# Performance work log

Hardware: AMD Instinct MI355X
Metric: run time of the kernel (lower is better)

## Reference

```python
import jax, jax.numpy as jnp
import numpy as np

B, T, D, MP = 32, 256, 512, 20


def setup_inputs() -> dict:
    key = jax.random.key(0)
    k1, k2, k3 = jax.random.split(key, 3)
    reps_lt = jax.random.normal(k1, (B, T, D), dtype=jnp.float32)
    reps_rt = jax.random.normal(k2, (B, T, D), dtype=jnp.float32)
    kernel = jax.random.normal(k3, (1, 1, 1, MP, D), dtype=jnp.float32)
    return {"reps_lt": reps_lt, "reps_rt": reps_rt, "kernel": kernel}


def reference(reps_lt, reps_rt, kernel):
    # kernel: (1,1,1,m,d) -> (m,d)
    km = kernel.reshape(kernel.shape[-2], kernel.shape[-1])
    # scores[b,t,s,m] = sum_d lt[b,t,d] * km[m,d] * rt[b,s,d]
    # matches original broadcast-multiply + sum over d (cosine_norm=False path)
    scores = jnp.einsum('btd,md,bsd->btsm', reps_lt, km, reps_rt)
    match = jnp.tanh(scores)               # [b, t1, t2, m]
    return jnp.max(match, axis=2)          # max-pool over t2 -> [b, t1, m]
```

## Files before the change

kernel.cpp:

```cpp
#include <hip/hip_runtime.h>


constexpr int TT = 256;
constexpr int DD = 512;
constexpr int NM = 20;
constexpr int NB = 32;
constexpr int BM = 128;
constexpr int BN = 256;
constexpr int BK = 32;
constexpr int NK = DD / BK;

typedef short bf16x8 __attribute__((ext_vector_type(8)));
typedef float f32x4  __attribute__((ext_vector_type(4)));

__device__ __forceinline__ void async_ld16(const void* g, void* l) {
    __builtin_amdgcn_global_load_lds(
        (const __attribute__((address_space(1))) void*)g,
        (__attribute__((address_space(3))) void*)l, 16, 0, 0);
}

__device__ __forceinline__ unsigned pack_bf16(float lo, float hi) {
    unsigned ulo = __builtin_bit_cast(unsigned, lo);
    unsigned uhi = __builtin_bit_cast(unsigned, hi);
    return (ulo >> 16) | (uhi & 0xFFFF0000u);
}

__device__ __forceinline__ unsigned mulpack(unsigned a2, float k0, float k1) {
    float f0 = __builtin_bit_cast(float, a2 << 16) * k0;
    float f1 = __builtin_bit_cast(float, a2 & 0xFFFF0000u) * k1;
    return __builtin_amdgcn_perm(__builtin_bit_cast(unsigned, f1),
                                 __builtin_bit_cast(unsigned, f0), 0x07060302u);
}

__global__ __launch_bounds__(256)
void cast_bf16(const float* __restrict__ lt, const float* __restrict__ rt,
               unsigned short* __restrict__ ltb, unsigned short* __restrict__ rtb)
{
    const int half = (int)gridDim.x >> 1;
    int bid = blockIdx.x;
    const float* src;
    unsigned short* dst;
    if (bid < half) { src = lt; dst = ltb; }
    else            { src = rt; dst = rtb; bid -= half; }
    size_t base = ((size_t)bid * 256 + threadIdx.x) * 8;
    float4 a = *(const float4*)(src + base);
    float4 b = *(const float4*)(src + base + 4);
    uint4 w;
    w.x = pack_bf16(a.x, a.y);
    w.y = pack_bf16(a.z, a.w);
    w.z = pack_bf16(b.x, b.y);
    w.w = pack_bf16(b.z, b.w);
    *(uint4*)(dst + base) = w;
}

__global__ __launch_bounds__(256, 2)
void mp_match_main(const unsigned short* __restrict__ ltb, const unsigned short* __restrict__ rtb,
                   const float* __restrict__ km, float* __restrict__ out)
{
    __shared__ __attribute__((aligned(16))) unsigned short Bsh[2][BN * 4 * 8];
    __shared__ __attribute__((aligned(16))) unsigned short Ash[2][BM * 4 * 8];
    __shared__ __attribute__((aligned(16))) float kmf[DD];
    __shared__ __attribute__((aligned(16))) float maxbuf[2][BM];

    const int f = blockIdx.x;
    const int c8 = f & 7;
    const int i = f >> 3;
    const int b = c8 + 8 * (i / 40);
    const int j = i % 40;
    const int m = j >> 1;
    const int t0 = (j & 1) * BM;

    const int tid  = threadIdx.x;
    const int w    = tid >> 6;
    const int lane = tid & 63;
    const int l15  = lane & 15;
    const int l4   = lane >> 4;
    const int wt   = (w & 1) * 64;
    const int wsi  = w >> 1;

    kmf[tid]       = km[(size_t)m * DD + tid];
    kmf[tid + 256] = km[(size_t)m * DD + tid + 256];

    const unsigned short* ltB = ltb + ((size_t)b * TT + t0) * DD;
    const unsigned short* rtB = rtb + (size_t)b * TT * DD;

    const int ar0 = tid >> 2,        ac = tid & 3;
    const int ar1 = (tid + 256) >> 2;
    const int ap0 = ac ^ ((ar0 >> 1) & 3);
    const int ap1 = ac ^ ((ar1 >> 1) & 3);
    const unsigned short* aSrc0 = ltB + (size_t)ar0 * DD + ac * 8;
    const unsigned short* aSrc1 = ltB + (size_t)ar1 * DD + ac * 8;

    auto issueB = [&](int kk, int buf) {
        const int kb = kk * BK;
#pragma unroll
        for (int q = 0; q < 4; ++q) {
            int slot = q * 256 + tid;
            int row = slot >> 2;
            int c = (slot & 3) ^ ((slot >> 3) & 3);
            async_ld16(rtB + (size_t)row * DD + kb + c * 8,
                       (char*)&Bsh[buf][0] + (size_t)slot * 16);
        }
    };
    auto aload = [&](int kk, uint4* ar) {
        ar[0] = *(const uint4*)(aSrc0 + kk * BK);
        ar[1] = *(const uint4*)(aSrc1 + kk * BK);
    };
    auto scaleWrite = [&](int kk, int buf, const uint4* ar) {
        float4 k0 = *(const float4*)&kmf[kk * BK + ac * 8];
        float4 k1 = *(const float4*)&kmf[kk * BK + ac * 8 + 4];
        uint4 o;
        o.x = mulpack(ar[0].x, k0.x, k0.y);
        o.y = mulpack(ar[0].y, k0.z, k0.w);
        o.z = mulpack(ar[0].z, k1.x, k1.y);
        o.w = mulpack(ar[0].w, k1.z, k1.w);
        *(uint4*)&Ash[buf][(size_t)(ar0 * 4 + ap0) * 8] = o;
        o.x = mulpack(ar[1].x, k0.x, k0.y);
        o.y = mulpack(ar[1].y, k0.z, k0.w);
        o.z = mulpack(ar[1].z, k1.x, k1.y);
        o.w = mulpack(ar[1].w, k1.z, k1.w);
        *(uint4*)&Ash[buf][(size_t)(ar1 * 4 + ap1) * 8] = o;
    };

    f32x4 acc[4][8] = {};
    uint4 ar[2];

    aload(0, ar);
    issueB(0, 0);
    __syncthreads();
    scaleWrite(0, 0, ar);

    const int fpos = l4 ^ ((l15 >> 1) & 3);

    for (int kk = 0; kk < NK; ++kk) {
        const int buf = kk & 1;
        __syncthreads();
        if (kk + 1 < NK) {
            aload(kk + 1, ar);
            issueB(kk + 1, buf ^ 1);
        }
        bf16x8 af[4], bv[8];
#pragma unroll
        for (int ii = 0; ii < 4; ++ii)
            af[ii] = *(const bf16x8*)&Ash[buf][(size_t)((wt + ii * 16 + l15) * 4 + fpos) * 8];
#pragma unroll
        for (int jj = 0; jj < 8; ++jj)
            bv[jj] = *(const bf16x8*)&Bsh[buf][(size_t)((wsi * 128 + jj * 16 + l15) * 4 + fpos) * 8];
#pragma unroll
        for (int ii = 0; ii < 4; ++ii)
#pragma unroll
            for (int jj = 0; jj < 8; ++jj)
                acc[ii][jj] = __builtin_amdgcn_mfma_f32_16x16x32_bf16(af[ii], bv[jj], acc[ii][jj], 0, 0, 0);
        if (kk + 1 < NK)
            scaleWrite(kk + 1, buf ^ 1, ar);
    }

#pragma unroll
    for (int ii = 0; ii < 4; ++ii) {
        f32x4 v = acc[ii][0];
#pragma unroll
        for (int jj = 1; jj < 8; ++jj) {
            v.x = fmaxf(v.x, acc[ii][jj].x);
            v.y = fmaxf(v.y, acc[ii][jj].y);
            v.z = fmaxf(v.z, acc[ii][jj].z);
            v.w = fmaxf(v.w, acc[ii][jj].w);
        }
#pragma unroll
        for (int off = 1; off < 16; off <<= 1) {
            v.x = fmaxf(v.x, __shfl_xor(v.x, off, 64));
            v.y = fmaxf(v.y, __shfl_xor(v.y, off, 64));
            v.z = fmaxf(v.z, __shfl_xor(v.z, off, 64));
            v.w = fmaxf(v.w, __shfl_xor(v.w, off, 64));
        }
        if (l15 == 0)
            *(f32x4*)&maxbuf[wsi][wt + ii * 16 + l4 * 4] = v;
    }
    __syncthreads();
    if (tid < BM) {
        float v = fmaxf(maxbuf[0][tid], maxbuf[1][tid]);
        out[((size_t)b * TT + t0 + tid) * NM + m] = tanhf(v);
    }
}

__global__ __launch_bounds__(256, 2)
void mp_match_kernel(const float* __restrict__ lt, const float* __restrict__ rt,
                     const float* __restrict__ km, float* __restrict__ out)
{
    __shared__ __attribute__((aligned(16))) unsigned short Ash[2][4][BM][8];
    __shared__ __attribute__((aligned(16))) unsigned short Bsh2[2][4][BN][8];
    __shared__ __attribute__((aligned(16))) float maxbuf[2][BM];

    const int ttile = blockIdx.x, m = blockIdx.y, b = blockIdx.z;
    const int t0 = ttile * BM;
    const int tid = threadIdx.x, wave = tid >> 6, lane = tid & 63;
    const int l15 = lane & 15, l4 = lane >> 4;
    const int wt = (wave & 1) * 64, wsi = wave >> 1;

    const float* ltp = lt + ((size_t)b * TT + t0) * DD;
    const float* rtp = rt + (size_t)b * TT * DD;
    const float* kmp = km + (size_t)m * DD;
    const int a_t = tid >> 1, a_h = tid & 1;

    f32x4 acc[4][8] = {};

    auto stage = [&](int kk, int buf) {
        const int d0 = kk * BK;
        const float* ap = ltp + (size_t)a_t * DD + d0 + a_h * 16;
        const float* kp = kmp + d0 + a_h * 16;
#pragma unroll
        for (int q = 0; q < 2; ++q) {
            float4 x0 = *(const float4*)(ap + q * 8);
            float4 x1 = *(const float4*)(ap + q * 8 + 4);
            float4 k0 = *(const float4*)(kp + q * 8);
            float4 k1 = *(const float4*)(kp + q * 8 + 4);
            uint4 wv;
            wv.x = pack_bf16(x0.x * k0.x, x0.y * k0.y);
            wv.y = pack_bf16(x0.z * k0.z, x0.w * k0.w);
            wv.z = pack_bf16(x1.x * k1.x, x1.y * k1.y);
            wv.w = pack_bf16(x1.z * k1.z, x1.w * k1.w);
            *(uint4*)&Ash[buf][a_h * 2 + q][a_t][0] = wv;
        }
        const float* bp = rtp + (size_t)tid * DD + d0;
#pragma unroll
        for (int p = 0; p < 4; ++p) {
            float4 y0 = *(const float4*)(bp + p * 8);
            float4 y1 = *(const float4*)(bp + p * 8 + 4);
            uint4 wv;
            wv.x = pack_bf16(y0.x, y0.y);
            wv.y = pack_bf16(y0.z, y0.w);
            wv.z = pack_bf16(y1.x, y1.y);
            wv.w = pack_bf16(y1.z, y1.w);
            *(uint4*)&Bsh2[buf][p][tid][0] = wv;
        }
    };

    stage(0, 0);
    for (int kk = 0; kk < NK; ++kk) {
        const int buf = kk & 1;
        __syncthreads();
        bf16x8 af[4], bfv[8];
#pragma unroll
        for (int i = 0; i < 4; ++i)
            af[i] = *(const bf16x8*)&Ash[buf][l4][wt + i * 16 + l15][0];
#pragma unroll
        for (int j = 0; j < 8; ++j)
            bfv[j] = *(const bf16x8*)&Bsh2[buf][l4][wsi * 128 + j * 16 + l15][0];
        if (kk + 1 < NK) stage(kk + 1, buf ^ 1);
#pragma unroll
        for (int i = 0; i < 4; ++i)
#pragma unroll
            for (int j = 0; j < 8; ++j)
                acc[i][j] = __builtin_amdgcn_mfma_f32_16x16x32_bf16(af[i], bfv[j], acc[i][j], 0, 0, 0);
    }
#pragma unroll
    for (int i = 0; i < 4; ++i) {
        f32x4 v = acc[i][0];
#pragma unroll
        for (int j = 1; j < 8; ++j) {
            v.x = fmaxf(v.x, acc[i][j].x); v.y = fmaxf(v.y, acc[i][j].y);
            v.z = fmaxf(v.z, acc[i][j].z); v.w = fmaxf(v.w, acc[i][j].w);
        }
#pragma unroll
        for (int off = 1; off < 16; off <<= 1) {
            v.x = fmaxf(v.x, __shfl_xor(v.x, off, 64));
            v.y = fmaxf(v.y, __shfl_xor(v.y, off, 64));
            v.z = fmaxf(v.z, __shfl_xor(v.z, off, 64));
            v.w = fmaxf(v.w, __shfl_xor(v.w, off, 64));
        }
        if (l15 == 0) *(f32x4*)&maxbuf[wsi][wt + i * 16 + l4 * 4] = v;
    }
    __syncthreads();
    if (tid < BM) {
        float v = fmaxf(maxbuf[0][tid], maxbuf[1][tid]);
        out[((size_t)b * TT + t0 + tid) * NM + m] = tanhf(v);
    }
}

extern "C" void kernel_launch(void* const* d_in, const int* in_sizes, int n_in,
                              void* d_out, int out_size, void* d_ws, size_t ws_size,
                              hipStream_t stream) {
    const float* lt  = (const float*)d_in[0];
    const float* rt  = (const float*)d_in[1];
    const float* km  = (const float*)d_in[2];
    float*       out = (float*)d_out;

    const size_t elems = (size_t)NB * TT * DD;
    const size_t need  = 2 * elems * sizeof(unsigned short);

    if (ws_size >= need) {
        unsigned short* ltb = (unsigned short*)d_ws;
        unsigned short* rtb = ltb + elems;
        const int cast_blocks_per_tensor = (int)(elems / (8 * 256));
        cast_bf16<<<cast_blocks_per_tensor * 2, 256, 0, stream>>>(lt, rt, ltb, rtb);
        mp_match_main<<<dim3(1280), 256, 0, stream>>>(ltb, rtb, km, out);
    } else {
        mp_match_kernel<<<dim3(TT / BM, NM, NB), 256, 0, stream>>>(lt, rt, km, out);
    }
}
```

Measured before the change: 133.6 us.

## Split s-dimension across two blocks with partial max buffer and combine kernel

Adds a split kernel that tiles the s axis into two 128-row halves, so each block computes a 128x128 tile with smaller LDS and fewer accumulators, launching 2560 blocks at occupancy 3. Partial maxima go to a workspace buffer, and a small combine kernel takes the max of the two halves and applies tanh. The aim is more parallelism and occupancy. The cost is an extra kernel launch, a partial-result write and read, and duplicate A-tile loads and scaling per block.

```diff
diff --git a/kernel.cpp b/kernel.cpp
--- a/kernel.cpp
+++ b/kernel.cpp
@@ -53,22 +53,24 @@
     *(uint4*)(dst + base) = w;
 }
 
-__global__ __launch_bounds__(256, 2)
-void mp_match_main(const unsigned short* __restrict__ ltb, const unsigned short* __restrict__ rtb,
-                   const float* __restrict__ km, float* __restrict__ out)
+__global__ __launch_bounds__(256, 3)
+void mp_match_split(const unsigned short* __restrict__ ltb, const unsigned short* __restrict__ rtb,
+                    const float* __restrict__ km, float* __restrict__ part)
 {
-    __shared__ __attribute__((aligned(16))) unsigned short Bsh[2][BN * 4 * 8];
     __shared__ __attribute__((aligned(16))) unsigned short Ash[2][BM * 4 * 8];
+    __shared__ __attribute__((aligned(16))) unsigned short Bsh[2][BM * 4 * 8];
     __shared__ __attribute__((aligned(16))) float kmf[DD];
     __shared__ __attribute__((aligned(16))) float maxbuf[2][BM];
 
-    const int f = blockIdx.x;
+    const int f  = blockIdx.x;
     const int c8 = f & 7;
-    const int i = f >> 3;
-    const int b = c8 + 8 * (i / 40);
-    const int j = i % 40;
-    const int m = j >> 1;
-    const int t0 = (j & 1) * BM;
+    const int i  = f >> 3;
+    const int b  = c8 + 8 * (i / 80);
+    const int j  = i % 80;
+    const int m  = j >> 2;
+    const int t0 = ((j >> 1) & 1) * 128;
+    const int s0 = (j & 1) * 128;
+    const int sT = j & 1;
 
     const int tid  = threadIdx.x;
     const int w    = tid >> 6;
@@ -76,13 +78,13 @@
     const int l15  = lane & 15;
     const int l4   = lane >> 4;
     const int wt   = (w & 1) * 64;
-    const int wsi  = w >> 1;
+    const int wsO  = (w >> 1) * 64;
 
     kmf[tid]       = km[(size_t)m * DD + tid];
     kmf[tid + 256] = km[(size_t)m * DD + tid + 256];
 
     const unsigned short* ltB = ltb + ((size_t)b * TT + t0) * DD;
-    const unsigned short* rtB = rtb + (size_t)b * TT * DD;
+    const unsigned short* rtB = rtb + ((size_t)b * TT + s0) * DD;
 
     const int ar0 = tid >> 2,        ac = tid & 3;
     const int ar1 = (tid + 256) >> 2;
@@ -94,7 +96,7 @@
     auto issueB = [&](int kk, int buf) {
         const int kb = kk * BK;
 #pragma unroll
-        for (int q = 0; q < 4; ++q) {
+        for (int q = 0; q < 2; ++q) {
             int slot = q * 256 + tid;
             int row = slot >> 2;
             int c = (slot & 3) ^ ((slot >> 3) & 3);
@@ -122,6 +124,143 @@
         *(uint4*)&Ash[buf][(size_t)(ar1 * 4 + ap1) * 8] = o;
     };
 
+    f32x4 acc[4][4] = {};
+    uint4 ar[2];
+
+    aload(0, ar);
+    issueB(0, 0);
+    __syncthreads();
+    scaleWrite(0, 0, ar);
+
+    const int fpos = l4 ^ ((l15 >> 1) & 3);
+
+    for (int kk = 0; kk < NK; ++kk) {
+        const int buf = kk & 1;
+        __syncthreads();
+        if (kk + 1 < NK) {
+            aload(kk + 1, ar);
+            issueB(kk + 1, buf ^ 1);
+        }
+        bf16x8 af[4], bv[4];
+#pragma unroll
+        for (int ii = 0; ii < 4; ++ii)
+            af[ii] = *(const bf16x8*)&Ash[buf][(size_t)((wt + ii * 16 + l15) * 4 + fpos) * 8];
+#pragma unroll
+        for (int jj = 0; jj < 4; ++jj)
+            bv[jj] = *(const bf16x8*)&Bsh[buf][(size_t)((wsO + jj * 16 + l15) * 4 + fpos) * 8];
+#pragma unroll
+        for (int ii = 0; ii < 4; ++ii)
+#pragma unroll
+            for (int jj = 0; jj < 4; ++jj)
+                acc[ii][jj] = __builtin_amdgcn_mfma_f32_16x16x32_bf16(af[ii], bv[jj], acc[ii][jj], 0, 0, 0);
+        if (kk + 1 < NK)
+            scaleWrite(kk + 1, buf ^ 1, ar);
+    }
+
+#pragma unroll
+    for (int ii = 0; ii < 4; ++ii) {
+        f32x4 v = acc[ii][0];
+#pragma unroll
+        for (int jj = 1; jj < 4; ++jj) {
+            v.x = fmaxf(v.x, acc[ii][jj].x);
+            v.y = fmaxf(v.y, acc[ii][jj].y);
+            v.z = fmaxf(v.z, acc[ii][jj].z);
+            v.w = fmaxf(v.w, acc[ii][jj].w);
+        }
+#pragma unroll
+        for (int off = 1; off < 16; off <<= 1) {
+            v.x = fmaxf(v.x, __shfl_xor(v.x, off, 64));
+            v.y = fmaxf(v.y, __shfl_xor(v.y, off, 64));
+            v.z = fmaxf(v.z, __shfl_xor(v.z, off, 64));
+            v.w = fmaxf(v.w, __shfl_xor(v.w, off, 64));
+        }
+        if (l15 == 0)
+            *(f32x4*)&maxbuf[w >> 1][wt + ii * 16 + l4 * 4] = v;
+    }
+    __syncthreads();
+    if (tid < BM) {
+        float v = fmaxf(maxbuf[0][tid], maxbuf[1][tid]);
+        part[(((size_t)sT * NB + b) * TT + t0 + tid) * NM + m] = v;
+    }
+}
+
+__global__ __launch_bounds__(256)
+void mp_combine(const float* __restrict__ part, float* __restrict__ out, int n)
+{
+    int idx = blockIdx.x * 256 + threadIdx.x;
+    if (idx < n)
+        out[idx] = tanhf(fmaxf(part[idx], part[(size_t)n + idx]));
+}
+
+__global__ __launch_bounds__(256, 2)
+void mp_match_main(const unsigned short* __restrict__ ltb, const unsigned short* __restrict__ rtb,
+                   const float* __restrict__ km, float* __restrict__ out)
+{
+    __shared__ __attribute__((aligned(16))) unsigned short Bsh[2][BN * 4 * 8];
+    __shared__ __attribute__((aligned(16))) unsigned short Ash[2][BM * 4 * 8];
+    __shared__ __attribute__((aligned(16))) float kmf[DD];
+    __shared__ __attribute__((aligned(16))) float maxbuf[2][BM];
+
+    const int f = blockIdx.x;
+    const int c8 = f & 7;
+    const int i = f >> 3;
+    const int b = c8 + 8 * (i / 40);
+    const int j = i % 40;
+    const int m = j >> 1;
+    const int t0 = (j & 1) * BM;
+
+    const int tid  = threadIdx.x;
+    const int w    = tid >> 6;
+    const int lane = tid & 63;
+    const int l15  = lane & 15;
+    const int l4   = lane >> 4;
+    const int wt   = (w & 1) * 64;
+    const int wsi  = w >> 1;
+
+    kmf[tid]       = km[(size_t)m * DD + tid];
+    kmf[tid + 256] = km[(size_t)m * DD + tid + 256];
+
+    const unsigned short* ltB = ltb + ((size_t)b * TT + t0) * DD;
+    const unsigned short* rtB = rtb + (size_t)b * TT * DD;
+
+    const int ar0 = tid >> 2,        ac = tid & 3;
+    const int ar1 = (tid + 256) >> 2;
+    const int ap0 = ac ^ ((ar0 >> 1) & 3);
+    const int ap1 = ac ^ ((ar1 >> 1) & 3);
+    const unsigned short* aSrc0 = ltB + (size_t)ar0 * DD + ac * 8;
+    const unsigned short* aSrc1 = ltB + (size_t)ar1 * DD + ac * 8;
+
+    auto issueB = [&](int kk, int buf) {
+        const int kb = kk * BK;
+#pragma unroll
+        for (int q = 0; q < 4; ++q) {
+            int slot = q * 256 + tid;
+            int row = slot >> 2;
+            int c = (slot & 3) ^ ((slot >> 3) & 3);
+            async_ld16(rtB + (size_t)row * DD + kb + c * 8,
+                       (char*)&Bsh[buf][0] + (size_t)slot * 16);
+        }
+    };
+    auto aload = [&](int kk, uint4* ar) {
+        ar[0] = *(const uint4*)(aSrc0 + kk * BK);
+        ar[1] = *(const uint4*)(aSrc1 + kk * BK);
+    };
+    auto scaleWrite = [&](int kk, int buf, const uint4* ar) {
+        float4 k0 = *(const float4*)&kmf[kk * BK + ac * 8];
+        float4 k1 = *(const float4*)&kmf[kk * BK + ac * 8 + 4];
+        uint4 o;
+        o.x = mulpack(ar[0].x, k0.x, k0.y);
+        o.y = mulpack(ar[0].y, k0.z, k0.w);
+        o.z = mulpack(ar[0].z, k1.x, k1.y);
+        o.w = mulpack(ar[0].w, k1.z, k1.w);
+        *(uint4*)&Ash[buf][(size_t)(ar0 * 4 + ap0) * 8] = o;
+        o.x = mulpack(ar[1].x, k0.x, k0.y);
+        o.y = mulpack(ar[1].y, k0.z, k0.w);
+        o.z = mulpack(ar[1].z, k1.x, k1.y);
+        o.w = mulpack(ar[1].w, k1.z, k1.w);
+        *(uint4*)&Ash[buf][(size_t)(ar1 * 4 + ap1) * 8] = o;
+    };
+
     f32x4 acc[4][8] = {};
     uint4 ar[2];
 
@@ -285,14 +424,22 @@
     float*       out = (float*)d_out;
 
     const size_t elems = (size_t)NB * TT * DD;
-    const size_t need  = 2 * elems * sizeof(unsigned short);
-
-    if (ws_size >= need) {
+    const size_t castB = 2 * elems * sizeof(unsigned short);
+    const int    nOut  = NB * TT * NM;
+    const size_t partB = 2 * (size_t)nOut * sizeof(float);
+
+    if (ws_size >= castB + partB) {
         unsigned short* ltb = (unsigned short*)d_ws;
         unsigned short* rtb = ltb + elems;
-        const int cast_blocks_per_tensor = (int)(elems / (8 * 256));
-        cast_bf16<<<cast_blocks_per_tensor * 2, 256, 0, stream>>>(lt, rt, ltb, rtb);
-        mp_match_main<<<dim3(1280), 256, 0, stream>>>(ltb, rtb, km, out);
+        float* part = (float*)((char*)d_ws + castB);
+        cast_bf16<<<4096, 256, 0, stream>>>(lt, rt, ltb, rtb);
+        mp_match_split<<<2560, 256, 0, stream>>>(ltb, rtb, km, part);
+        mp_combine<<<(nOut + 255) / 256, 256, 0, stream>>>(part, out, nOut);
+    } else if (ws_size >= castB) {
+        unsigned short* ltb = (unsigned short*)d_ws;
+        unsigned short* rtb = ltb + elems;
+        cast_bf16<<<4096, 256, 0, stream>>>(lt, rt, ltb, rtb);
+        mp_match_main<<<1280, 256, 0, stream>>>(ltb, rtb, km, out);
     } else {
         mp_match_kernel<<<dim3(TT / BM, NM, NB), 256, 0, stream>>>(lt, rt, km, out);
     }
```

Result: no change. 133.0 us (-0.4%).

## Halve M tile to 64 rows and raise occupancy to three blocks per CU

Applied to the files above, without the earlier changes.

Shrinks the lt row tile from 128 to 64, which doubles the grid to 2560 blocks. Each wave now owns a 64x64 output sub-tile (4x4 MFMA accumulators) instead of 64x128, and the final max reduces over four waves. Launch bounds are raised to 3 blocks per CU to use the lower register and LDS footprint. The goal is better latency hiding and load balance across CUs. The cost is that every rt tile is streamed twice as often and there are fewer MFMAs per LDS read.

```diff
diff --git a/kernel.cpp b/kernel.cpp
--- a/kernel.cpp
+++ b/kernel.cpp
@@ -5,7 +5,7 @@
 constexpr int DD = 512;
 constexpr int NM = 20;
 constexpr int NB = 32;
-constexpr int BM = 128;
+constexpr int BM = 64;
 constexpr int BN = 256;
 constexpr int BK = 32;
 constexpr int NK = DD / BK;
@@ -53,30 +53,29 @@
     *(uint4*)(dst + base) = w;
 }
 
-__global__ __launch_bounds__(256, 2)
+__global__ __launch_bounds__(256, 3)
 void mp_match_main(const unsigned short* __restrict__ ltb, const unsigned short* __restrict__ rtb,
                    const float* __restrict__ km, float* __restrict__ out)
 {
     __shared__ __attribute__((aligned(16))) unsigned short Bsh[2][BN * 4 * 8];
     __shared__ __attribute__((aligned(16))) unsigned short Ash[2][BM * 4 * 8];
     __shared__ __attribute__((aligned(16))) float kmf[DD];
-    __shared__ __attribute__((aligned(16))) float maxbuf[2][BM];
-
-    const int f = blockIdx.x;
+    __shared__ __attribute__((aligned(16))) float maxbuf[4][BM];
+
+    const int f  = blockIdx.x;
     const int c8 = f & 7;
-    const int i = f >> 3;
-    const int b = c8 + 8 * (i / 40);
-    const int j = i % 40;
-    const int m = j >> 1;
-    const int t0 = (j & 1) * BM;
+    const int i  = f >> 3;
+    const int b  = c8 + 8 * (i / 80);
+    const int j  = i % 80;
+    const int m  = j >> 2;
+    const int t0 = (j & 3) * BM;
 
     const int tid  = threadIdx.x;
     const int w    = tid >> 6;
     const int lane = tid & 63;
     const int l15  = lane & 15;
     const int l4   = lane >> 4;
-    const int wt   = (w & 1) * 64;
-    const int wsi  = w >> 1;
+    const int wsO  = w * 64;
 
     kmf[tid]       = km[(size_t)m * DD + tid];
     kmf[tid + 256] = km[(size_t)m * DD + tid + 256];
@@ -84,12 +83,9 @@
     const unsigned short* ltB = ltb + ((size_t)b * TT + t0) * DD;
     const unsigned short* rtB = rtb + (size_t)b * TT * DD;
 
-    const int ar0 = tid >> 2,        ac = tid & 3;
-    const int ar1 = (tid + 256) >> 2;
-    const int ap0 = ac ^ ((ar0 >> 1) & 3);
-    const int ap1 = ac ^ ((ar1 >> 1) & 3);
-    const unsigned short* aSrc0 = ltB + (size_t)ar0 * DD + ac * 8;
-    const unsigned short* aSrc1 = ltB + (size_t)ar1 * DD + ac * 8;
+    const int arow = tid >> 2, ac = tid & 3;
+    const int apos = ac ^ ((arow >> 1) & 3);
+    const unsigned short* aSrc = ltB + (size_t)arow * DD + ac * 8;
 
     auto issueB = [&](int kk, int buf) {
         const int kb = kk * BK;
@@ -102,30 +98,21 @@
                        (char*)&Bsh[buf][0] + (size_t)slot * 16);
         }
     };
-    auto aload = [&](int kk, uint4* ar) {
-        ar[0] = *(const uint4*)(aSrc0 + kk * BK);
-        ar[1] = *(const uint4*)(aSrc1 + kk * BK);
-    };
-    auto scaleWrite = [&](int kk, int buf, const uint4* ar) {
+    auto scaleWrite = [&](int kk, int buf, uint4 a) {
         float4 k0 = *(const float4*)&kmf[kk * BK + ac * 8];
         float4 k1 = *(const float4*)&kmf[kk * BK + ac * 8 + 4];
         uint4 o;
-        o.x = mulpack(ar[0].x, k0.x, k0.y);
-        o.y = mulpack(ar[0].y, k0.z, k0.w);
-        o.z = mulpack(ar[0].z, k1.x, k1.y);
-        o.w = mulpack(ar[0].w, k1.z, k1.w);
-        *(uint4*)&Ash[buf][(size_t)(ar0 * 4 + ap0) * 8] = o;
-        o.x = mulpack(ar[1].x, k0.x, k0.y);
-        o.y = mulpack(ar[1].y, k0.z, k0.w);
-        o.z = mulpack(ar[1].z, k1.x, k1.y);
-        o.w = mulpack(ar[1].w, k1.z, k1.w);
-        *(uint4*)&Ash[buf][(size_t)(ar1 * 4 + ap1) * 8] = o;
+        o.x = mulpack(a.x, k0.x, k0.y);
+        o.y = mulpack(a.y, k0.z, k0.w);
+        o.z = mulpack(a.z, k1.x, k1.y);
+        o.w = mulpack(a.w, k1.z, k1.w);
+        *(uint4*)&Ash[buf][(size_t)(arow * 4 + apos) * 8] = o;
     };
 
-    f32x4 acc[4][8] = {};
-    uint4 ar[2];
-
-    aload(0, ar);
+    f32x4 acc[4][4] = {};
+    uint4 ar;
+
+    ar = *(const uint4*)(aSrc);
     issueB(0, 0);
     __syncthreads();
     scaleWrite(0, 0, ar);
@@ -136,20 +123,20 @@
         const int buf = kk & 1;
         __syncthreads();
         if (kk + 1 < NK) {
-            aload(kk + 1, ar);
+            ar = *(const uint4*)(aSrc + (kk + 1) * BK);
             issueB(kk + 1, buf ^ 1);
         }
-        bf16x8 af[4], bv[8];
+        bf16x8 af[4], bv[4];
 #pragma unroll
         for (int ii = 0; ii < 4; ++ii)
-            af[ii] = *(const bf16x8*)&Ash[buf][(size_t)((wt + ii * 16 + l15) * 4 + fpos) * 8];
-#pragma unroll
-        for (int jj = 0; jj < 8; ++jj)
-            bv[jj] = *(const bf16x8*)&Bsh[buf][(size_t)((wsi * 128 + jj * 16 + l15) * 4 + fpos) * 8];
+            af[ii] = *(const bf16x8*)&Ash[buf][(size_t)((ii * 16 + l15) * 4 + fpos) * 8];
+#pragma unroll
+        for (int jj = 0; jj < 4; ++jj)
+            bv[jj] = *(const bf16x8*)&Bsh[buf][(size_t)((wsO + jj * 16 + l15) * 4 + fpos) * 8];
 #pragma unroll
         for (int ii = 0; ii < 4; ++ii)
 #pragma unroll
-            for (int jj = 0; jj < 8; ++jj)
+            for (int jj = 0; jj < 4; ++jj)
                 acc[ii][jj] = __builtin_amdgcn_mfma_f32_16x16x32_bf16(af[ii], bv[jj], acc[ii][jj], 0, 0, 0);
         if (kk + 1 < NK)
             scaleWrite(kk + 1, buf ^ 1, ar);
@@ -159,7 +146,7 @@
     for (int ii = 0; ii < 4; ++ii) {
         f32x4 v = acc[ii][0];
 #pragma unroll
-        for (int jj = 1; jj < 8; ++jj) {
+        for (int jj = 1; jj < 4; ++jj) {
             v.x = fmaxf(v.x, acc[ii][jj].x);
             v.y = fmaxf(v.y, acc[ii][jj].y);
             v.z = fmaxf(v.z, acc[ii][jj].z);
@@ -173,11 +160,12 @@
             v.w = fmaxf(v.w, __shfl_xor(v.w, off, 64));
         }
         if (l15 == 0)
-            *(f32x4*)&maxbuf[wsi][wt + ii * 16 + l4 * 4] = v;
+            *(f32x4*)&maxbuf[w][ii * 16 + l4 * 4] = v;
     }
     __syncthreads();
     if (tid < BM) {
-        float v = fmaxf(maxbuf[0][tid], maxbuf[1][tid]);
+        float v = fmaxf(fmaxf(maxbuf[0][tid], maxbuf[1][tid]),
+                        fmaxf(maxbuf[2][tid], maxbuf[3][tid]));
         out[((size_t)b * TT + t0 + tid) * NM + m] = tanhf(v);
     }
 }
@@ -186,12 +174,12 @@
 void mp_match_kernel(const float* __restrict__ lt, const float* __restrict__ rt,
                      const float* __restrict__ km, float* __restrict__ out)
 {
-    __shared__ __attribute__((aligned(16))) unsigned short Ash[2][4][BM][8];
+    __shared__ __attribute__((aligned(16))) unsigned short Ash[2][4][128][8];
     __shared__ __attribute__((aligned(16))) unsigned short Bsh2[2][4][BN][8];
-    __shared__ __attribute__((aligned(16))) float maxbuf[2][BM];
+    __shared__ __attribute__((aligned(16))) float maxbuf[2][128];
 
     const int ttile = blockIdx.x, m = blockIdx.y, b = blockIdx.z;
-    const int t0 = ttile * BM;
+    const int t0 = ttile * 128;
     const int tid = threadIdx.x, wave = tid >> 6, lane = tid & 63;
     const int l15 = lane & 15, l4 = lane >> 4;
     const int wt = (wave & 1) * 64, wsi = wave >> 1;
@@ -270,7 +258,7 @@
         if (l15 == 0) *(f32x4*)&maxbuf[wsi][wt + i * 16 + l4 * 4] = v;
     }
     __syncthreads();
-    if (tid < BM) {
+    if (tid < 128) {
         float v = fmaxf(maxbuf[0][tid], maxbuf[1][tid]);
         out[((size_t)b * TT + t0 + tid) * NM + m] = tanhf(v);
     }
@@ -285,15 +273,14 @@
     float*       out = (float*)d_out;
 
     const size_t elems = (size_t)NB * TT * DD;
-    const size_t need  = 2 * elems * sizeof(unsigned short);
-
-    if (ws_size >= need) {
+    const size_t castB = 2 * elems * sizeof(unsigned short);
+
+    if (ws_size >= castB) {
         unsigned short* ltb = (unsigned short*)d_ws;
         unsigned short* rtb = ltb + elems;
-        const int cast_blocks_per_tensor = (int)(elems / (8 * 256));
-        cast_bf16<<<cast_blocks_per_tensor * 2, 256, 0, stream>>>(lt, rt, ltb, rtb);
-        mp_match_main<<<dim3(1280), 256, 0, stream>>>(ltb, rtb, km, out);
+        cast_bf16<<<4096, 256, 0, stream>>>(lt, rt, ltb, rtb);
+        mp_match_main<<<2560, 256, 0, stream>>>(ltb, rtb, km, out);
     } else {
-        mp_match_kernel<<<dim3(TT / BM, NM, NB), 256, 0, stream>>>(lt, rt, km, out);
-    }
-}
+        mp_match_kernel<<<dim3(2, NM, NB), 256, 0, stream>>>(lt, rt, km, out);
+    }
+}
```

After: 139.6 us. 4.5% more time.

## Split s-dimension across blocks and combine partial maxima in separate kernel

Applied to the files above, without the earlier changes.

The main matmul-max kernel now tiles the s (rt) dimension in halves of 128, doubling the grid to 2560 smaller blocks with a 4x4 accumulator tile per wave and launch bounds raised to 4 blocks per CU. Partial maxima go to workspace and a new combine kernel takes the max of the two halves and applies tanh. This aims for more occupancy and better load balance across CUs. In exchange the A tile and its per-m scaling are loaded and computed twice, MFMA reuse per LDS load drops, and there is an extra launch and workspace round trip.

```diff
diff --git a/kernel.cpp b/kernel.cpp
--- a/kernel.cpp
+++ b/kernel.cpp
@@ -6,7 +6,6 @@
 constexpr int NM = 20;
 constexpr int NB = 32;
 constexpr int BM = 128;
-constexpr int BN = 256;
 constexpr int BK = 32;
 constexpr int NK = DD / BK;
 
@@ -53,22 +52,24 @@
     *(uint4*)(dst + base) = w;
 }
 
-__global__ __launch_bounds__(256, 2)
-void mp_match_main(const unsigned short* __restrict__ ltb, const unsigned short* __restrict__ rtb,
-                   const float* __restrict__ km, float* __restrict__ out)
+__global__ __launch_bounds__(256, 4)
+void mp_match_split(const unsigned short* __restrict__ ltb, const unsigned short* __restrict__ rtb,
+                    const float* __restrict__ km, float* __restrict__ part)
 {
-    __shared__ __attribute__((aligned(16))) unsigned short Bsh[2][BN * 4 * 8];
     __shared__ __attribute__((aligned(16))) unsigned short Ash[2][BM * 4 * 8];
+    __shared__ __attribute__((aligned(16))) unsigned short Bsh[2][BM * 4 * 8];
     __shared__ __attribute__((aligned(16))) float kmf[DD];
     __shared__ __attribute__((aligned(16))) float maxbuf[2][BM];
 
-    const int f = blockIdx.x;
+    const int f  = blockIdx.x;
     const int c8 = f & 7;
-    const int i = f >> 3;
-    const int b = c8 + 8 * (i / 40);
-    const int j = i % 40;
-    const int m = j >> 1;
-    const int t0 = (j & 1) * BM;
+    const int i  = f >> 3;
+    const int b  = c8 + 8 * (i / 80);
+    const int j  = i % 80;
+    const int m  = j >> 2;
+    const int t0 = ((j >> 1) & 1) * 128;
+    const int s0 = (j & 1) * 128;
+    const int sT = j & 1;
 
     const int tid  = threadIdx.x;
     const int w    = tid >> 6;
@@ -76,13 +77,13 @@
     const int l15  = lane & 15;
     const int l4   = lane >> 4;
     const int wt   = (w & 1) * 64;
-    const int wsi  = w >> 1;
+    const int wsO  = (w >> 1) * 64;
 
     kmf[tid]       = km[(size_t)m * DD + tid];
     kmf[tid + 256] = km[(size_t)m * DD + tid + 256];
 
     const unsigned short* ltB = ltb + ((size_t)b * TT + t0) * DD;
-    const unsigned short* rtB = rtb + (size_t)b * TT * DD;
+    const unsigned short* rtB = rtb + ((size_t)b * TT + s0) * DD;
 
     const int ar0 = tid >> 2,        ac = tid & 3;
     const int ar1 = (tid + 256) >> 2;
@@ -94,7 +95,7 @@
     auto issueB = [&](int kk, int buf) {
         const int kb = kk * BK;
 #pragma unroll
-        for (int q = 0; q < 4; ++q) {
+        for (int q = 0; q < 2; ++q) {
             int slot = q * 256 + tid;
             int row = slot >> 2;
             int c = (slot & 3) ^ ((slot >> 3) & 3);
@@ -122,7 +123,7 @@
         *(uint4*)&Ash[buf][(size_t)(ar1 * 4 + ap1) * 8] = o;
     };
 
-    f32x4 acc[4][8] = {};
+    f32x4 acc[4][4] = {};
     uint4 ar[2];
 
     aload(0, ar);
@@ -139,17 +140,17 @@
             aload(kk + 1, ar);
             issueB(kk + 1, buf ^ 1);
         }
-        bf16x8 af[4], bv[8];
+        bf16x8 af[4], bv[4];
 #pragma unroll
         for (int ii = 0; ii < 4; ++ii)
             af[ii] = *(const bf16x8*)&Ash[buf][(size_t)((wt + ii * 16 + l15) * 4 + fpos) * 8];
 #pragma unroll
-        for (int jj = 0; jj < 8; ++jj)
-            bv[jj] = *(const bf16x8*)&Bsh[buf][(size_t)((wsi * 128 + jj * 16 + l15) * 4 + fpos) * 8];
+        for (int jj = 0; jj < 4; ++jj)
+            bv[jj] = *(const bf16x8*)&Bsh[buf][(size_t)((wsO + jj * 16 + l15) * 4 + fpos) * 8];
 #pragma unroll
         for (int ii = 0; ii < 4; ++ii)
 #pragma unroll
-            for (int jj = 0; jj < 8; ++jj)
+            for (int jj = 0; jj < 4; ++jj)
                 acc[ii][jj] = __builtin_amdgcn_mfma_f32_16x16x32_bf16(af[ii], bv[jj], acc[ii][jj], 0, 0, 0);
         if (kk + 1 < NK)
             scaleWrite(kk + 1, buf ^ 1, ar);
@@ -159,7 +160,7 @@
     for (int ii = 0; ii < 4; ++ii) {
         f32x4 v = acc[ii][0];
 #pragma unroll
-        for (int jj = 1; jj < 8; ++jj) {
+        for (int jj = 1; jj < 4; ++jj) {
             v.x = fmaxf(v.x, acc[ii][jj].x);
             v.y = fmaxf(v.y, acc[ii][jj].y);
             v.z = fmaxf(v.z, acc[ii][jj].z);
@@ -173,25 +174,33 @@
             v.w = fmaxf(v.w, __shfl_xor(v.w, off, 64));
         }
         if (l15 == 0)
-            *(f32x4*)&maxbuf[wsi][wt + ii * 16 + l4 * 4] = v;
+            *(f32x4*)&maxbuf[w >> 1][wt + ii * 16 + l4 * 4] = v;
     }
     __syncthreads();
     if (tid < BM) {
         float v = fmaxf(maxbuf[0][tid], maxbuf[1][tid]);
-        out[((size_t)b * TT + t0 + tid) * NM + m] = tanhf(v);
-    }
+        part[(((size_t)sT * NB + b) * TT + t0 + tid) * NM + m] = v;
+    }
+}
+
+__global__ __launch_bounds__(256)
+void mp_combine(const float* __restrict__ part, float* __restrict__ out, int n)
+{
+    int idx = blockIdx.x * 256 + threadIdx.x;
+    if (idx < n)
+        out[idx] = tanhf(fmaxf(part[idx], part[(size_t)n + idx]));
 }
 
 __global__ __launch_bounds__(256, 2)
 void mp_match_kernel(const float* __restrict__ lt, const float* __restrict__ rt,
                      const float* __restrict__ km, float* __restrict__ out)
 {
-    __shared__ __attribute__((aligned(16))) unsigned short Ash[2][4][BM][8];
-    __shared__ __attribute__((aligned(16))) unsigned short Bsh2[2][4][BN][8];
-    __shared__ __attribute__((aligned(16))) float maxbuf[2][BM];
+    __shared__ __attribute__((aligned(16))) unsigned short Ash[2][4][128][8];
+    __shared__ __attribute__((aligned(16))) unsigned short Bsh2[2][4][256][8];
+    __shared__ __attribute__((aligned(16))) float maxbuf[2][128];
 
     const int ttile = blockIdx.x, m = blockIdx.y, b = blockIdx.z;
-    const int t0 = ttile * BM;
+    const int t0 = ttile * 128;
     const int tid = threadIdx.x, wave = tid >> 6, lane = tid & 63;
     const int l15 = lane & 15, l4 = lane >> 4;
     const int wt = (wave & 1) * 64, wsi = wave >> 1;
@@ -270,7 +279,7 @@
         if (l15 == 0) *(f32x4*)&maxbuf[wsi][wt + i * 16 + l4 * 4] = v;
     }
     __syncthreads();
-    if (tid < BM) {
+    if (tid < 128) {
         float v = fmaxf(maxbuf[0][tid], maxbuf[1][tid]);
         out[((size_t)b * TT + t0 + tid) * NM + m] = tanhf(v);
     }
@@ -285,15 +294,18 @@
     float*       out = (float*)d_out;
 
     const size_t elems = (size_t)NB * TT * DD;
-    const size_t need  = 2 * elems * sizeof(unsigned short);
-
-    if (ws_size >= need) {
+    const size_t castB = 2 * elems * sizeof(unsigned short);
+    const int    nOut  = NB * TT * NM;
+    const size_t partB = 2 * (size_t)nOut * sizeof(float);
+
+    if (ws_size >= castB + partB) {
         unsigned short* ltb = (unsigned short*)d_ws;
         unsigned short* rtb = ltb + elems;
-        const int cast_blocks_per_tensor = (int)(elems / (8 * 256));
-        cast_bf16<<<cast_blocks_per_tensor * 2, 256, 0, stream>>>(lt, rt, ltb, rtb);
-        mp_match_main<<<dim3(1280), 256, 0, stream>>>(ltb, rtb, km, out);
+        float* part = (float*)((char*)d_ws + castB);
+        cast_bf16<<<4096, 256, 0, stream>>>(lt, rt, ltb, rtb);
+        mp_match_split<<<2560, 256, 0, stream>>>(ltb, rtb, km, part);
+        mp_combine<<<(nOut + 255) / 256, 256, 0, stream>>>(part, out, nOut);
     } else {
-        mp_match_kernel<<<dim3(TT / BM, NM, NB), 256, 0, stream>>>(lt, rt, km, out);
-    }
-}
+        mp_match_kernel<<<dim3(2, NM, NB), 256, 0, stream>>>(lt, rt, km, out);
+    }
+}
```

Result: no change. 133.9 us (+0.3%).
